# Optimization experiments

Measured on AMD Instinct MI355X. Metric: run time of the kernel, lower is better.

The kernel has to match this reference:

```python
import jax, jax.numpy as jnp
import numpy as np

B, C, H, W = 16, 512, 32, 32
GROUPS = 8
EPS = 1e-5


def setup_inputs() -> dict:
    key = jax.random.key(0)
    ks = jax.random.split(key, 7)
    s = 1.0 / np.sqrt(C)
    return {
        "x": jax.random.normal(ks[0], (B, C, H, W), dtype=jnp.float32),
        "gamma": jnp.ones((C,), dtype=jnp.float32),
        "beta": jnp.zeros((C,), dtype=jnp.float32),
        "w_qkv": jax.random.normal(ks[1], (3 * C, C), dtype=jnp.float32) * s,
        "b_qkv": jnp.zeros((3 * C,), dtype=jnp.float32),
        "w_proj": jax.random.normal(ks[2], (C, C), dtype=jnp.float32) * s,
        "b_proj": jnp.zeros((C,), dtype=jnp.float32),
    }


def group_norm(x, gamma, beta):
    b, c, h, w = x.shape
    xg = x.reshape(b, GROUPS, c // GROUPS, h, w)
    mean = xg.mean(axis=(2, 3, 4), keepdims=True)
    var = xg.var(axis=(2, 3, 4), keepdims=True)
    xn = ((xg - mean) * jax.lax.rsqrt(var + EPS)).reshape(b, c, h, w)
    return xn * gamma[None, :, None, None] + beta[None, :, None, None]


def reference(x, gamma, beta, w_qkv, b_qkv, w_proj, b_proj):
    b, c, h, w = x.shape
    n = h * w
    hn = group_norm(x, gamma, beta)
    # 1x1 conv == channel matmul: [3C, C] x [B, C, N] -> [B, 3C, N]
    qkv = jnp.einsum('oc,bcn->bon', w_qkv, hn.reshape(b, c, n)) + b_qkv[None, :, None]
    q, k, v = jnp.split(qkv, 3, axis=1)  # each [B, C, N]
    scale = c ** (-0.5)
    # scores [B, N, N]: q^T k
    attn = jax.nn.softmax(jnp.einsum('bcn,bcm->bnm', q, k) * scale, axis=-1)
    out = jnp.einsum('bnm,bcm->bcn', attn, v)  # [B, C, N]
    proj = jnp.einsum('oc,bcn->bon', w_proj, out) + b_proj[None, :, None]
    return x + proj.reshape(b, c, h, w)
```

## Files before the change

### kernel.cpp

```cpp
#include <hip/hip_runtime.h>


#define BATCH 16
#define CCH 512
#define NSP 1024
#define EPSV 1e-5f
#define BK 32

typedef short bf16x8 __attribute__((ext_vector_type(8)));
typedef float f32x4 __attribute__((ext_vector_type(4)));

__device__ __forceinline__ unsigned short f2bf(float f) {
    unsigned int u = __float_as_uint(f);
    u += 0x7FFF + ((u >> 16) & 1);
    return (unsigned short)(u >> 16);
}

__device__ __forceinline__ void glds16(const void* g, void* l) {
    __builtin_amdgcn_global_load_lds(
        (const __attribute__((address_space(1))) unsigned int*)g,
        (__attribute__((address_space(3))) unsigned int*)l, 16, 0, 0);
}

__device__ __forceinline__ void gemm128_loop(
    const unsigned short* __restrict__ Ag, const unsigned short* __restrict__ Bg,
    int astr, int bstr, int ktot, short* Al, short* Bl, f32x4* acc) {
    const int t = threadIdx.x;
    const int w = t >> 6, lane = t & 63;
    const int wr = (w >> 1) * 64, wc = (w & 1) * 64;
    const int fr = lane & 15, fko = (lane >> 4) * 8;
    const int r0 = t >> 2;
    const int kc = (t & 3) * 8;
    short* Alb0 = Al + w * 512;
    short* Alb1 = Al + 2048 + w * 512;
    short* Blb0 = Bl + w * 512;
    short* Blb1 = Bl + 2048 + w * 512;
    for (int k0 = 0; k0 < ktot; k0 += BK) {
        glds16(Ag + (size_t)r0 * astr + k0 + kc, Alb0);
        glds16(Ag + (size_t)(r0 + 64) * astr + k0 + kc, Alb1);
        glds16(Bg + (size_t)r0 * bstr + k0 + kc, Blb0);
        glds16(Bg + (size_t)(r0 + 64) * bstr + k0 + kc, Blb1);
        __syncthreads();
        bf16x8 af[4], bfr[4];
#pragma unroll
        for (int mi = 0; mi < 4; mi++)
            af[mi] = *(const bf16x8*)(Al + (wr + mi * 16 + fr) * BK + fko);
#pragma unroll
        for (int ni = 0; ni < 4; ni++)
            bfr[ni] = *(const bf16x8*)(Bl + (wc + ni * 16 + fr) * BK + fko);
#pragma unroll
        for (int mi = 0; mi < 4; mi++)
#pragma unroll
            for (int ni = 0; ni < 4; ni++)
                acc[mi * 4 + ni] = __builtin_amdgcn_mfma_f32_16x16x32_bf16(
                    af[mi], bfr[ni], acc[mi * 4 + ni], 0, 0, 0);
        __syncthreads();
    }
}

#define EPI_SETUP()                                          \
    const int t = threadIdx.x, lane = t & 63, w = t >> 6;    \
    const int wr = (w >> 1) * 64, wc = (w & 1) * 64;         \
    const int fr = lane & 15, rr0 = (lane >> 4) * 4;

#define ACC_INIT(acc)                                        \
    f32x4 acc[16];                                           \
    _Pragma("unroll") for (int i = 0; i < 16; i++)           \
        acc[i] = (f32x4){0.f, 0.f, 0.f, 0.f};

__global__ __launch_bounds__(256) void cvt_bf16_k(
    const float* __restrict__ a, unsigned short* __restrict__ oa, int na4,
    const float* __restrict__ b, unsigned short* __restrict__ ob, int nb4) {
    int i = blockIdx.x * 256 + threadIdx.x;
    const float* src;
    unsigned short* dst;
    int j;
    if (i < na4) { src = a; dst = oa; j = i; }
    else { j = i - na4; if (j >= nb4) return; src = b; dst = ob; }
    float4 v = ((const float4*)src)[j];
    ushort4 o;
    o.x = f2bf(v.x); o.y = f2bf(v.y); o.z = f2bf(v.z); o.w = f2bf(v.w);
    ((ushort4*)dst)[j] = o;
}

__global__ __launch_bounds__(256) void gn_stats_k(
    const float* __restrict__ x, float* __restrict__ stats) {
    const int bg = blockIdx.x;
    const float4* xp = (const float4*)(x + (size_t)bg * 65536);
    const int t = threadIdx.x;
    float s = 0.f, q = 0.f;
#pragma unroll
    for (int i = 0; i < 64; i++) {
        float4 v = xp[t + i * 256];
        s += v.x + v.y + v.z + v.w;
        q += v.x * v.x + v.y * v.y + v.z * v.z + v.w * v.w;
    }
#pragma unroll
    for (int off = 32; off; off >>= 1) {
        s += __shfl_down(s, off);
        q += __shfl_down(q, off);
    }
    __shared__ float rs[4], rq[4];
    const int wave = t >> 6, lane = t & 63;
    if (lane == 0) { rs[wave] = s; rq[wave] = q; }
    __syncthreads();
    if (t == 0) {
        float S = rs[0] + rs[1] + rs[2] + rs[3];
        float Q = rq[0] + rq[1] + rq[2] + rq[3];
        const float inv = 1.f / 65536.f;
        float mean = S * inv;
        float var = Q * inv - mean * mean;
        stats[bg * 2] = mean;
        stats[bg * 2 + 1] = rsqrtf(var + EPSV);
    }
}

__global__ __launch_bounds__(256) void gn_tr_k(
    const float* __restrict__ x, const float* __restrict__ gamma,
    const float* __restrict__ beta, const float* __restrict__ stats,
    unsigned short* __restrict__ hn_t) {
    const int nt = blockIdx.x, ct = blockIdx.y, b = blockIdx.z;
    __shared__ __align__(16) unsigned short T[64 * 72];
    const int t = threadIdx.x;
    const float mean = stats[(b * 8 + ct) * 2];
    const float rstd = stats[(b * 8 + ct) * 2 + 1];
    const int cl = t >> 2, nc = t & 3;
    const int c = ct * 64 + cl;
    const float ga = gamma[c] * rstd;
    const float be = beta[c] - mean * ga;
    const float4* xp = (const float4*)(x + ((size_t)b * CCH + c) * NSP + nt * 64);
#pragma unroll
    for (int j = 0; j < 4; j++) {
        float4 v = xp[nc * 4 + j];
        int n = nc * 16 + j * 4;
        T[(n + 0) * 72 + cl] = f2bf(v.x * ga + be);
        T[(n + 1) * 72 + cl] = f2bf(v.y * ga + be);
        T[(n + 2) * 72 + cl] = f2bf(v.z * ga + be);
        T[(n + 3) * 72 + cl] = f2bf(v.w * ga + be);
    }
    __syncthreads();
    const int nl = t >> 2, cc = t & 3;
    unsigned short* dst = hn_t + ((size_t)b * NSP + nt * 64 + nl) * CCH + ct * 64 + cc * 16;
    const unsigned short* src = T + nl * 72 + cc * 16;
    *(uint4*)dst = *(const uint4*)src;
    *(uint4*)(dst + 8) = *(const uint4*)(src + 8);
}

__global__ __launch_bounds__(256) void gemm_qkv_k(
    const unsigned short* __restrict__ hn_t, const unsigned short* __restrict__ wq,
    const float* __restrict__ bq, unsigned short* __restrict__ QKt,
    unsigned short* __restrict__ Vb) {
    __shared__ __align__(16) short Al[128 * BK], Bl[128 * BK];
    const int ntc = blockIdx.x * 128, y = blockIdx.y, b = blockIdx.z;
    ACC_INIT(acc);
    if (y < 8) {
        const int mt = y * 128;
        gemm128_loop(hn_t + ((size_t)b * NSP + mt) * CCH,
                     wq + (size_t)ntc * CCH, CCH, CCH, CCH, Al, Bl, acc);
        unsigned short* Ob = QKt + (size_t)b * NSP * 1024;
        EPI_SETUP();
#pragma unroll
        for (int ni = 0; ni < 4; ni++) {
            int col = ntc + wc + ni * 16 + fr;
            float bias = bq[col];
#pragma unroll
            for (int mi = 0; mi < 4; mi++) {
                int row = mt + wr + mi * 16 + rr0;
#pragma unroll
                for (int r = 0; r < 4; r++)
                    Ob[(size_t)(row + r) * 1024 + col] = f2bf(acc[mi * 4 + ni][r] + bias);
            }
        }
    } else {
        const int mt = (y - 8) * 128;
        gemm128_loop(wq + (size_t)(1024 + mt) * CCH,
                     hn_t + ((size_t)b * NSP + ntc) * CCH, CCH, CCH, CCH, Al, Bl, acc);
        unsigned short* Ob = Vb + (size_t)b * CCH * NSP;
        EPI_SETUP();
#pragma unroll
        for (int mi = 0; mi < 4; mi++) {
            int row = mt + wr + mi * 16 + rr0;
#pragma unroll
            for (int r = 0; r < 4; r++) {
                float bias = bq[1024 + row + r];
#pragma unroll
                for (int ni = 0; ni < 4; ni++) {
                    int col = ntc + wc + ni * 16 + fr;
                    Ob[(size_t)(row + r) * NSP + col] = f2bf(acc[mi * 4 + ni][r] + bias);
                }
            }
        }
    }
}

__global__ __launch_bounds__(256) void gemm_scores_k(
    const unsigned short* __restrict__ QKt, unsigned short* __restrict__ expS,
    float* __restrict__ Lsum) {
    __shared__ __align__(16) short Al[128 * BK], Bl[128 * BK];
    const int nt = blockIdx.x * 128, mt = blockIdx.y * 128, b = blockIdx.z;
    const unsigned short* base = QKt + (size_t)b * NSP * 1024;
    ACC_INIT(acc);
    gemm128_loop(base + (size_t)mt * 1024, base + (size_t)nt * 1024 + 512,
                 1024, 1024, 512, Al, Bl, acc);
    unsigned short* Ob = expS + (size_t)b * NSP * NSP;
    float* Ls = Lsum + (size_t)b * NSP;
    const float scale = 0.044194173824159216f;
    EPI_SETUP();
#pragma unroll
    for (int mi = 0; mi < 4; mi++) {
#pragma unroll
        for (int r = 0; r < 4; r++) {
            const int row = mt + wr + mi * 16 + rr0 + r;
            float rs = 0.f;
#pragma unroll
            for (int ni = 0; ni < 4; ni++) {
                int col = nt + wc + ni * 16 + fr;
                float e = __expf(acc[mi * 4 + ni][r] * scale);
                Ob[(size_t)row * NSP + col] = f2bf(e);
                rs += e;
            }
            rs += __shfl_xor(rs, 1);
            rs += __shfl_xor(rs, 2);
            rs += __shfl_xor(rs, 4);
            rs += __shfl_xor(rs, 8);
            if (fr == 0) atomicAdd(&Ls[row], rs);
        }
    }
}

__global__ __launch_bounds__(256) void gemm_pv_k(
    const unsigned short* __restrict__ expS, const unsigned short* __restrict__ Vb,
    const float* __restrict__ Lsum, unsigned short* __restrict__ At) {
    __shared__ __align__(16) short Al[128 * BK], Bl[128 * BK];
    const int ntc = blockIdx.x * 128, mt = blockIdx.y * 128, b = blockIdx.z;
    ACC_INIT(acc);
    gemm128_loop(expS + ((size_t)b * NSP + mt) * NSP,
                 Vb + ((size_t)b * CCH + ntc) * NSP, NSP, NSP, NSP, Al, Bl, acc);
    unsigned short* Ob = At + (size_t)b * NSP * CCH;
    const float* Ls = Lsum + (size_t)b * NSP;
    EPI_SETUP();
#pragma unroll
    for (int mi = 0; mi < 4; mi++) {
        int row = mt + wr + mi * 16 + rr0;
#pragma unroll
        for (int r = 0; r < 4; r++) {
            float inv = __builtin_amdgcn_rcpf(Ls[row + r]);
#pragma unroll
            for (int ni = 0; ni < 4; ni++) {
                int col = ntc + wc + ni * 16 + fr;
                Ob[(size_t)(row + r) * CCH + col] = f2bf(acc[mi * 4 + ni][r] * inv);
            }
        }
    }
}

__global__ __launch_bounds__(256) void gemm_proj_k(
    const unsigned short* __restrict__ At, const unsigned short* __restrict__ wp,
    const float* __restrict__ bp, const float* __restrict__ x,
    float* __restrict__ out) {
    __shared__ __align__(16) short Al[128 * BK], Bl[128 * BK];
    const int nt = blockIdx.x * 128, mt = blockIdx.y * 128, b = blockIdx.z;
    ACC_INIT(acc);
    gemm128_loop(wp + (size_t)mt * CCH, At + ((size_t)b * NSP + nt) * CCH,
                 CCH, CCH, CCH, Al, Bl, acc);
    const size_t bbase = (size_t)b * CCH * NSP;
    EPI_SETUP();
#pragma unroll
    for (int mi = 0; mi < 4; mi++) {
        int row = mt + wr + mi * 16 + rr0;
#pragma unroll
        for (int r = 0; r < 4; r++) {
            float bias = bp[row + r];
#pragma unroll
            for (int ni = 0; ni < 4; ni++) {
                int col = nt + wc + ni * 16 + fr;
                size_t idx = bbase + (size_t)(row + r) * NSP + col;
                out[idx] = x[idx] + bias + acc[mi * 4 + ni][r];
            }
        }
    }
}

extern "C" void kernel_launch(void* const* d_in, const int* in_sizes, int n_in,
                              void* d_out, int out_size, void* d_ws, size_t ws_size,
                              hipStream_t stream) {
    const float* x = (const float*)d_in[0];
    const float* gamma = (const float*)d_in[1];
    const float* beta = (const float*)d_in[2];
    const float* w_qkv = (const float*)d_in[3];
    const float* b_qkv = (const float*)d_in[4];
    const float* w_proj = (const float*)d_in[5];
    const float* b_proj = (const float*)d_in[6];
    float* out = (float*)d_out;

    char* ws = (char*)d_ws;
    const size_t MB = 1048576;
    unsigned short* wqkv_bf = (unsigned short*)ws;
    unsigned short* wproj_bf = (unsigned short*)(ws + 1572864);
    float* stats = (float*)(ws + 2 * MB);
    float* Lsum = (float*)(ws + 2 * MB + 65536);
    unsigned short* hn_t = (unsigned short*)(ws + 4 * MB);
    unsigned short* At = hn_t;
    unsigned short* QKt = (unsigned short*)(ws + 24 * MB);
    unsigned short* Vb = (unsigned short*)(ws + 60 * MB);
    unsigned short* expS = (unsigned short*)(ws + 80 * MB);

    hipMemsetAsync(Lsum, 0, BATCH * NSP * sizeof(float), stream);
    cvt_bf16_k<<<1024, 256, 0, stream>>>(w_qkv, wqkv_bf, 196608, w_proj, wproj_bf, 65536);
    gn_stats_k<<<128, 256, 0, stream>>>(x, stats);
    gn_tr_k<<<dim3(16, 8, BATCH), 256, 0, stream>>>(x, gamma, beta, stats, hn_t);
    gemm_qkv_k<<<dim3(8, 12, BATCH), 256, 0, stream>>>(hn_t, wqkv_bf, b_qkv, QKt, Vb);
    gemm_scores_k<<<dim3(8, 8, BATCH), 256, 0, stream>>>(QKt, expS, Lsum);
    gemm_pv_k<<<dim3(4, 8, BATCH), 256, 0, stream>>>(expS, Vb, Lsum, At);
    gemm_proj_k<<<dim3(8, 4, BATCH), 256, 0, stream>>>(At, wproj_bf, b_proj, x, out);
}
```

Before: 240.0 us.

## Remap GEMM grids so each batch stays on one XCD; merge setup kernels

Flattens the grids of the four GEMM kernels to 1-D and decodes block ids so that all tiles of a batch go to the same XCD (blockIdx & 7 picks the batch, split in two halves). The aim is to keep each batch's operands in that XCD's L2 and improve reuse. It also fuses the GroupNorm stats kernel and the weight bf16 conversion into one launch to save a kernel launch. This relies on round-robin XCD dispatch of workgroups, and it may hurt load balance if that dispatch assumption does not hold.

```diff
diff --git a/kernel.cpp b/kernel.cpp
--- a/kernel.cpp
+++ b/kernel.cpp
@@ -21,6 +21,16 @@
         (const __attribute__((address_space(1))) unsigned int*)g,
         (__attribute__((address_space(3))) unsigned int*)l, 16, 0, 0);
 }
+
+#define XCD_MAP(GX_LOG2, PER, xv, yv, bv)                 \
+    const int lin_ = blockIdx.x;                          \
+    const int xcd_ = lin_ & 7;                            \
+    int slot_ = lin_ >> 3;                                \
+    const int hi_ = (slot_ >= (PER)) ? 1 : 0;             \
+    const int bv = xcd_ + 8 * hi_;                        \
+    slot_ -= hi_ * (PER);                                 \
+    const int xv = slot_ & ((1 << (GX_LOG2)) - 1);        \
+    const int yv = slot_ >> (GX_LOG2);
 
 __device__ __forceinline__ void gemm128_loop(
     const unsigned short* __restrict__ Ag, const unsigned short* __restrict__ Bg,
@@ -68,50 +78,50 @@
     _Pragma("unroll") for (int i = 0; i < 16; i++)           \
         acc[i] = (f32x4){0.f, 0.f, 0.f, 0.f};
 
-__global__ __launch_bounds__(256) void cvt_bf16_k(
-    const float* __restrict__ a, unsigned short* __restrict__ oa, int na4,
-    const float* __restrict__ b, unsigned short* __restrict__ ob, int nb4) {
-    int i = blockIdx.x * 256 + threadIdx.x;
-    const float* src;
-    unsigned short* dst;
-    int j;
-    if (i < na4) { src = a; dst = oa; j = i; }
-    else { j = i - na4; if (j >= nb4) return; src = b; dst = ob; }
-    float4 v = ((const float4*)src)[j];
-    ushort4 o;
-    o.x = f2bf(v.x); o.y = f2bf(v.y); o.z = f2bf(v.z); o.w = f2bf(v.w);
-    ((ushort4*)dst)[j] = o;
-}
-
-__global__ __launch_bounds__(256) void gn_stats_k(
-    const float* __restrict__ x, float* __restrict__ stats) {
-    const int bg = blockIdx.x;
-    const float4* xp = (const float4*)(x + (size_t)bg * 65536);
+__global__ __launch_bounds__(256) void setup_k(
+    const float* __restrict__ x, float* __restrict__ stats,
+    const float* __restrict__ wa, unsigned short* __restrict__ oa, int na4,
+    const float* __restrict__ wb, unsigned short* __restrict__ ob, int nb4) {
     const int t = threadIdx.x;
-    float s = 0.f, q = 0.f;
-#pragma unroll
-    for (int i = 0; i < 64; i++) {
-        float4 v = xp[t + i * 256];
-        s += v.x + v.y + v.z + v.w;
-        q += v.x * v.x + v.y * v.y + v.z * v.z + v.w * v.w;
-    }
-#pragma unroll
-    for (int off = 32; off; off >>= 1) {
-        s += __shfl_down(s, off);
-        q += __shfl_down(q, off);
-    }
-    __shared__ float rs[4], rq[4];
-    const int wave = t >> 6, lane = t & 63;
-    if (lane == 0) { rs[wave] = s; rq[wave] = q; }
-    __syncthreads();
-    if (t == 0) {
-        float S = rs[0] + rs[1] + rs[2] + rs[3];
-        float Q = rq[0] + rq[1] + rq[2] + rq[3];
-        const float inv = 1.f / 65536.f;
-        float mean = S * inv;
-        float var = Q * inv - mean * mean;
-        stats[bg * 2] = mean;
-        stats[bg * 2 + 1] = rsqrtf(var + EPSV);
+    if (blockIdx.x < 128) {
+        const int bg = blockIdx.x;
+        const float4* xp = (const float4*)(x + (size_t)bg * 65536);
+        float s = 0.f, q = 0.f;
+#pragma unroll
+        for (int i = 0; i < 64; i++) {
+            float4 v = xp[t + i * 256];
+            s += v.x + v.y + v.z + v.w;
+            q += v.x * v.x + v.y * v.y + v.z * v.z + v.w * v.w;
+        }
+#pragma unroll
+        for (int off = 32; off; off >>= 1) {
+            s += __shfl_down(s, off);
+            q += __shfl_down(q, off);
+        }
+        __shared__ float rs[4], rq[4];
+        const int wave = t >> 6, lane = t & 63;
+        if (lane == 0) { rs[wave] = s; rq[wave] = q; }
+        __syncthreads();
+        if (t == 0) {
+            float S = rs[0] + rs[1] + rs[2] + rs[3];
+            float Q = rq[0] + rq[1] + rq[2] + rq[3];
+            const float inv = 1.f / 65536.f;
+            float mean = S * inv;
+            float var = Q * inv - mean * mean;
+            stats[bg * 2] = mean;
+            stats[bg * 2 + 1] = rsqrtf(var + EPSV);
+        }
+    } else {
+        int i = (blockIdx.x - 128) * 256 + t;
+        const float* src;
+        unsigned short* dst;
+        int j;
+        if (i < na4) { src = wa; dst = oa; j = i; }
+        else { j = i - na4; if (j >= nb4) return; src = wb; dst = ob; }
+        float4 v = ((const float4*)src)[j];
+        ushort4 o;
+        o.x = f2bf(v.x); o.y = f2bf(v.y); o.z = f2bf(v.z); o.w = f2bf(v.w);
+        ((ushort4*)dst)[j] = o;
     }
 }
 
@@ -151,7 +161,8 @@
     const float* __restrict__ bq, unsigned short* __restrict__ QKt,
     unsigned short* __restrict__ Vb) {
     __shared__ __align__(16) short Al[128 * BK], Bl[128 * BK];
-    const int ntc = blockIdx.x * 128, y = blockIdx.y, b = blockIdx.z;
+    XCD_MAP(3, 96, xb, y, b);
+    const int ntc = xb * 128;
     ACC_INIT(acc);
     if (y < 8) {
         const int mt = y * 128;
@@ -197,7 +208,8 @@
     const unsigned short* __restrict__ QKt, unsigned short* __restrict__ expS,
     float* __restrict__ Lsum) {
     __shared__ __align__(16) short Al[128 * BK], Bl[128 * BK];
-    const int nt = blockIdx.x * 128, mt = blockIdx.y * 128, b = blockIdx.z;
+    XCD_MAP(3, 64, xb, yb, b);
+    const int nt = xb * 128, mt = yb * 128;
     const unsigned short* base = QKt + (size_t)b * NSP * 1024;
     ACC_INIT(acc);
     gemm128_loop(base + (size_t)mt * 1024, base + (size_t)nt * 1024 + 512,
@@ -232,7 +244,8 @@
     const unsigned short* __restrict__ expS, const unsigned short* __restrict__ Vb,
     const float* __restrict__ Lsum, unsigned short* __restrict__ At) {
     __shared__ __align__(16) short Al[128 * BK], Bl[128 * BK];
-    const int ntc = blockIdx.x * 128, mt = blockIdx.y * 128, b = blockIdx.z;
+    XCD_MAP(2, 32, xb, yb, b);
+    const int ntc = xb * 128, mt = yb * 128;
     ACC_INIT(acc);
     gemm128_loop(expS + ((size_t)b * NSP + mt) * NSP,
                  Vb + ((size_t)b * CCH + ntc) * NSP, NSP, NSP, NSP, Al, Bl, acc);
@@ -259,7 +272,8 @@
     const float* __restrict__ bp, const float* __restrict__ x,
     float* __restrict__ out) {
     __shared__ __align__(16) short Al[128 * BK], Bl[128 * BK];
-    const int nt = blockIdx.x * 128, mt = blockIdx.y * 128, b = blockIdx.z;
+    XCD_MAP(3, 32, xb, yb, b);
+    const int nt = xb * 128, mt = yb * 128;
     ACC_INIT(acc);
     gemm128_loop(wp + (size_t)mt * CCH, At + ((size_t)b * NSP + nt) * CCH,
                  CCH, CCH, CCH, Al, Bl, acc);
@@ -306,11 +320,11 @@
     unsigned short* expS = (unsigned short*)(ws + 80 * MB);
 
     hipMemsetAsync(Lsum, 0, BATCH * NSP * sizeof(float), stream);
-    cvt_bf16_k<<<1024, 256, 0, stream>>>(w_qkv, wqkv_bf, 196608, w_proj, wproj_bf, 65536);
-    gn_stats_k<<<128, 256, 0, stream>>>(x, stats);
+    setup_k<<<1152, 256, 0, stream>>>(x, stats, w_qkv, wqkv_bf, 196608,
+                                      w_proj, wproj_bf, 65536);
     gn_tr_k<<<dim3(16, 8, BATCH), 256, 0, stream>>>(x, gamma, beta, stats, hn_t);
-    gemm_qkv_k<<<dim3(8, 12, BATCH), 256, 0, stream>>>(hn_t, wqkv_bf, b_qkv, QKt, Vb);
-    gemm_scores_k<<<dim3(8, 8, BATCH), 256, 0, stream>>>(QKt, expS, Lsum);
-    gemm_pv_k<<<dim3(4, 8, BATCH), 256, 0, stream>>>(expS, Vb, Lsum, At);
-    gemm_proj_k<<<dim3(8, 4, BATCH), 256, 0, stream>>>(At, wproj_bf, b_proj, x, out);
-}
+    gemm_qkv_k<<<1536, 256, 0, stream>>>(hn_t, wqkv_bf, b_qkv, QKt, Vb);
+    gemm_scores_k<<<1024, 256, 0, stream>>>(QKt, expS, Lsum);
+    gemm_pv_k<<<512, 256, 0, stream>>>(expS, Vb, Lsum, At);
+    gemm_proj_k<<<512, 256, 0, stream>>>(At, wproj_bf, b_proj, x, out);
+}
```

Measured after the change: 225.7 us. 6.0% less time.
